# Kernel tuning notes

Measured on AMD Instinct MI355X. Metric: run time of the kernel, lower is better.

The kernel has to match this reference:

```python
import jax, jax.numpy as jnp
import numpy as np

B, D, A, R = 256, 1024, 1024, 8  # batch, feat_dim, ada_dim, rank
I = A  # inter_dim defaults to ada_dim
LN_EPS = 1e-5


def setup_inputs() -> dict:
    key = jax.random.key(0)
    ks = jax.random.split(key, 5)
    return {
        "x": jax.random.normal(ks[0], (B, D), jnp.float32),
        "ada_emb": jax.random.normal(ks[1], (B, A), jnp.float32),
        "base_layer": jax.random.normal(ks[2], (D, D), jnp.float32) * 0.02,
        "ln_gamma": jnp.ones((A,), jnp.float32),
        "ln_beta": jnp.zeros((A,), jnp.float32),
        "W1": jax.random.normal(ks[3], (A, I), jnp.float32) * 0.02,
        "b1": jnp.zeros((I,), jnp.float32),
        "W2": jax.random.normal(ks[4], (I, D * R * 2), jnp.float32) * 0.02,
        "b2": jnp.zeros((D * R * 2,), jnp.float32),
    }


def reference(x, ada_emb, base_layer, ln_gamma, ln_beta, W1, b1, W2, b2):
    Bc, Dc = x.shape
    # norm_cond: LayerNorm over ada_dim
    mu = jnp.mean(ada_emb, axis=-1, keepdims=True)
    var = jnp.var(ada_emb, axis=-1, keepdims=True)
    cond = (ada_emb - mu) * jax.lax.rsqrt(var + LN_EPS) * ln_gamma + ln_beta
    # gen_weight: Linear -> GELU (exact, erf) -> Linear
    h = jax.nn.gelu(cond @ W1 + b1, approximate=False)
    w = h @ W2 + b2                      # [B, 2*D*R]
    x_a, x_b = jnp.split(w, 2, axis=-1)
    x_a = x_a.reshape(Bc, Dc, R)         # [B, D, R]
    x_b = x_b.reshape(Bc, Dc, R)         # [B, D, R]
    # per-sample low-rank weight added to the shared base layer
    layer = base_layer[None, :, :] + jnp.einsum('bdr,bkr->bdk', x_a, x_b)  # [B, D, D]
    out = jnp.einsum('bc,bco->bo', x, layer)
    return x + out  # residual=True
```

## Files before the change

### kernel.cpp

```cpp
#include <hip/hip_runtime.h>
#include <math.h>

#define BB 256
#define DD 1024
#define AA 1024
#define RR 8
#define II 1024
#define NOUT (2*DD*RR)
#define LN_EPS 1e-5f

typedef __attribute__((ext_vector_type(8))) short bf16x8;
typedef __attribute__((ext_vector_type(8))) unsigned short ushort8;
typedef __attribute__((ext_vector_type(4))) float f32x4;

typedef const __attribute__((address_space(1))) unsigned int gu32_t;
typedef __attribute__((address_space(3))) unsigned int lu32_t;

__device__ __forceinline__ void glds16(void* lds, const void* g) {
    __builtin_amdgcn_global_load_lds((gu32_t*)g, (lu32_t*)lds, 16, 0, 0);
}

__device__ __forceinline__ f32x4 mfma16(bf16x8 a, bf16x8 b, f32x4 c) {
    return __builtin_amdgcn_mfma_f32_16x16x32_bf16(a, b, c, 0, 0, 0);
}

__device__ __forceinline__ unsigned short f2bf(float x) {
    unsigned int u = __float_as_uint(x);
    unsigned int r = (u + 0x7fffu + ((u >> 16) & 1u)) >> 16;
    return (unsigned short)r;
}
__device__ __forceinline__ float bf2f(unsigned short b) {
    return __uint_as_float(((unsigned int)b) << 16);
}
__device__ __forceinline__ void split2(float x, unsigned short& hi, unsigned short& lo) {
    hi = f2bf(x);
    lo = f2bf(x - bf2f(hi));
}

__device__ __forceinline__ float gelu_exact(float v) {
    return 0.5f * v * (1.0f + erff(v * 0.70710678118654752f));
}

__global__ __launch_bounds__(256) void ln_split_kernel(const float* __restrict__ ada,
                                                       const float* __restrict__ xp,
                                                       const float* __restrict__ gamma,
                                                       const float* __restrict__ beta,
                                                       unsigned short* __restrict__ c_hi,
                                                       unsigned short* __restrict__ c_lo,
                                                       unsigned short* __restrict__ x_hi,
                                                       unsigned short* __restrict__ x_lo) {
    const int b = blockIdx.x;
    const int tid = threadIdx.x;
    const float4 v = ((const float4*)(ada + (size_t)b * AA))[tid];

    float s  = v.x + v.y + v.z + v.w;
    float ss = v.x * v.x + v.y * v.y + v.z * v.z + v.w * v.w;
    #pragma unroll
    for (int off = 32; off; off >>= 1) {
        s  += __shfl_down(s, off);
        ss += __shfl_down(ss, off);
    }
    __shared__ float red[2][4];
    const int wid = tid >> 6, lane = tid & 63;
    if (lane == 0) { red[0][wid] = s; red[1][wid] = ss; }
    __syncthreads();
    __shared__ float stats[2];
    if (tid == 0) {
        float S  = red[0][0] + red[0][1] + red[0][2] + red[0][3];
        float SS = red[1][0] + red[1][1] + red[1][2] + red[1][3];
        float mu  = S * (1.0f / AA);
        float var = SS * (1.0f / AA) - mu * mu;
        stats[0] = mu;
        stats[1] = rsqrtf(var + LN_EPS);
    }
    __syncthreads();
    const float mu = stats[0], inv = stats[1];
    const float4 g  = ((const float4*)gamma)[tid];
    const float4 be = ((const float4*)beta)[tid];
    float o[4];
    o[0] = (v.x - mu) * inv * g.x + be.x;
    o[1] = (v.y - mu) * inv * g.y + be.y;
    o[2] = (v.z - mu) * inv * g.z + be.z;
    o[3] = (v.w - mu) * inv * g.w + be.w;
    ushort4 H, L;
    split2(o[0], H.x, L.x); split2(o[1], H.y, L.y);
    split2(o[2], H.z, L.z); split2(o[3], H.w, L.w);
    ((ushort4*)(c_hi + (size_t)b * AA))[tid] = H;
    ((ushort4*)(c_lo + (size_t)b * AA))[tid] = L;

    const float4 xv = ((const float4*)(xp + (size_t)b * DD))[tid];
    split2(xv.x, H.x, L.x); split2(xv.y, H.y, L.y);
    split2(xv.z, H.z, L.z); split2(xv.w, H.w, L.w);
    ((ushort4*)(x_hi + (size_t)b * DD))[tid] = H;
    ((ushort4*)(x_lo + (size_t)b * DD))[tid] = L;
}

__global__ __launch_bounds__(256) void gemm_small(const unsigned short* __restrict__ x_hi,
                                                  const unsigned short* __restrict__ x_lo,
                                                  const unsigned short* __restrict__ c_hi,
                                                  const unsigned short* __restrict__ c_lo,
                                                  const float* __restrict__ base,
                                                  const float* __restrict__ W1,
                                                  const float* __restrict__ b1,
                                                  float* __restrict__ outy,
                                                  unsigned short* __restrict__ h_hi,
                                                  unsigned short* __restrict__ h_lo) {
    __shared__ __align__(16) unsigned short As[2][4096];
    __shared__ __align__(16) unsigned short Bs[2][8192];

    const int z = blockIdx.z;
    const unsigned short* __restrict__ Ahi = z ? c_hi : x_hi;
    const unsigned short* __restrict__ Alo = z ? c_lo : x_lo;
    const float* __restrict__ Bsrc = z ? W1 : base;

    const int tid = threadIdx.x;
    const int bn = blockIdx.x * 64;
    const int bm = blockIdx.y * 32;
    const int wid = tid >> 6, l = tid & 63;
    const int kg = l >> 4, lr16 = (l & 15) * 16;

    f32x4 acc[2];
    acc[0] = (f32x4)0.0f; acc[1] = (f32x4)0.0f;

    const int sn = tid & 63;
    const int s_nb = sn >> 4, s_l16 = (sn & 15) * 16;

    float v[2][8];

    #define SB_LOAD(K0)                                                          \
        _Pragma("unroll")                                                        \
        for (int h = 0; h < 2; h++) {                                            \
            const int c2 = (tid >> 6) * 2 + h;              \
            _Pragma("unroll")                                                    \
            for (int j = 0; j < 8; j++)                                          \
                v[h][j] = Bsrc[(size_t)((K0) + c2 * 8 + j) * 1024 + bn + sn];    \
        }

    #define SB_WRITE(BUF)                                                        \
        _Pragma("unroll")                                                        \
        for (int h = 0; h < 2; h++) {                                            \
            const int c2 = (tid >> 6) * 2 + h;                                   \
            ushort8 H, L;                                                        \
            _Pragma("unroll")                                                    \
            for (int j = 0; j < 8; j++) { unsigned short hh, ll;                 \
                split2(v[h][j], hh, ll); H[j] = hh; L[j] = ll; }                 \
            *(ushort8*)((char*)Bs[BUF] + ((0*4 + s_nb)*8 + c2)*256 + s_l16) = H; \
            *(ushort8*)((char*)Bs[BUF] + ((1*4 + s_nb)*8 + c2)*256 + s_l16) = L; \
        }

    #define SA_GLDS(BUF, K0)                                                     \
        _Pragma("unroll")                                                        \
        for (int c = 0; c < 2; c++) {                                            \
            const int ch = wid * 2 + c;                                \
            const int pl = ch >> 2, sub = ch & 3;                                \
            const int mb = sub >> 1, half = sub & 1;                             \
            const unsigned short* src = (pl ? Alo : Ahi)                         \
                + (size_t)(bm + mb * 16 + (l & 15)) * 1024 + (K0) + half * 32 + kg * 8; \
            glds16((char*)As[BUF] + (pl*2 + mb)*2048 + half*1024, src);          \
        }

    #define S_COMPUTE(BUF)                                                       \
        {                                                                        \
            _Pragma("unroll")                                                    \
            for (int s = 0; s < 2; s++) {                                        \
                bf16x8 a[2][2], bbf[2];                                          \
                _Pragma("unroll")                                                \
                for (int pl = 0; pl < 2; pl++) {                                 \
                    _Pragma("unroll")                                            \
                    for (int mi = 0; mi < 2; mi++)                               \
                        a[pl][mi] = *(const bf16x8*)((const char*)As[BUF] +      \
                            ((pl*2 + mi)*8 + s*4 + kg)*256 + lr16);              \
                    bbf[pl] = *(const bf16x8*)((const char*)Bs[BUF] +            \
                            ((pl*4 + wid)*8 + s*4 + kg)*256 + lr16);             \
                }                                                                \
                __builtin_amdgcn_s_setprio(1);                                   \
                _Pragma("unroll")                                                \
                for (int mi = 0; mi < 2; mi++) {                                 \
                    acc[mi] = mfma16(a[0][mi], bbf[0], acc[mi]);                 \
                    acc[mi] = mfma16(a[0][mi], bbf[1], acc[mi]);                 \
                    acc[mi] = mfma16(a[1][mi], bbf[0], acc[mi]);                 \
                }                                                                \
                __builtin_amdgcn_s_setprio(0);                                   \
            }                                                                    \
        }

    SB_LOAD(0);
    SA_GLDS(0, 0);
    SB_WRITE(0);
    __syncthreads();

    int cur = 0;
    for (int t = 0; t < 16; ++t) {
        if (t < 15) {
            const int k0n = (t + 1) * 64;
            SB_LOAD(k0n);
            SA_GLDS(cur ^ 1, k0n);
        }
        S_COMPUTE(cur);
        if (t < 15) {
            SB_WRITE(cur ^ 1);
        }
        __syncthreads();
        cur ^= 1;
    }

    #pragma unroll
    for (int mi = 0; mi < 2; mi++) {
        const int row0 = bm + mi * 16 + kg * 4;
        const int col  = bn + wid * 16 + (l & 15);
        #pragma unroll
        for (int j = 0; j < 4; j++) {
            float val = acc[mi][j];
            if (z == 0) {
                outy[(size_t)(row0 + j) * 1024 + col] = val;
            } else {
                float g = gelu_exact(val + b1[col]);
                unsigned short hi, lo;
                split2(g, hi, lo);
                h_hi[(size_t)(row0 + j) * 1024 + col] = hi;
                h_lo[(size_t)(row0 + j) * 1024 + col] = lo;
            }
        }
    }
    #undef SB_LOAD
    #undef SB_WRITE
    #undef SA_GLDS
    #undef S_COMPUTE
}

__global__ __launch_bounds__(256) void gemm_big(const unsigned short* __restrict__ Ahi,
                                                const unsigned short* __restrict__ Alo,
                                                const float* __restrict__ Bm,
                                                const float* __restrict__ bias,
                                                float* __restrict__ Cm) {
    __shared__ __align__(16) unsigned short As[2][8192];
    __shared__ __align__(16) unsigned short Bs[2][4096];

    const int orig = blockIdx.x;
    const int swz  = ((orig & 7) << 6) + (orig >> 3);
    const int bn = (swz >> 1) * 64;
    const int bm = (swz & 1) * 128;

    const int tid = threadIdx.x;
    const int wid = tid >> 6, l = tid & 63;
    const int wm = wid >> 1, wn = wid & 1;
    const int kg = l >> 4, lr16 = (l & 15) * 16;

    f32x4 acc[4][2];
    #pragma unroll
    for (int i = 0; i < 4; i++) { acc[i][0] = (f32x4)0.0f; acc[i][1] = (f32x4)0.0f; }

    const int sn = tid & 63;
    const int skc = tid >> 6;
    const int s_nb = sn >> 4, s_l16 = (sn & 15) * 16;

    float v[8];

    #define GB_LOAD(K0)                                                          \
        _Pragma("unroll")                                                        \
        for (int j = 0; j < 8; j++)                                              \
            v[j] = Bm[(size_t)((K0) + skc * 8 + j) * NOUT + bn + sn];

    #define GB_WRITE(BUF)                                                        \
        {                                                                        \
            ushort8 H, L;                                                        \
            _Pragma("unroll")                                                    \
            for (int j = 0; j < 8; j++) { unsigned short hh, ll;                 \
                split2(v[j], hh, ll); H[j] = hh; L[j] = ll; }                    \
            *(ushort8*)((char*)Bs[BUF] + ((0*4 + s_nb)*4 + skc)*256 + s_l16) = H;\
            *(ushort8*)((char*)Bs[BUF] + ((1*4 + s_nb)*4 + skc)*256 + s_l16) = L;\
        }

    #define GA_GLDS(BUF, K0)                                                     \
        _Pragma("unroll")                                                        \
        for (int c = 0; c < 4; c++) {                                            \
            const int ch = wid * 4 + c;                               \
            const int pl = ch >> 3, mb = ch & 7;                                 \
            const unsigned short* src = (pl ? Alo : Ahi)                         \
                + (size_t)(bm + mb * 16 + (l & 15)) * II + (K0) + kg * 8;        \
            glds16((char*)As[BUF] + ch * 1024, src);                             \
        }

    #define G_COMPUTE(BUF)                                                       \
        {                                                                        \
            bf16x8 a[2][4], bbf[2][2];                                           \
            _Pragma("unroll")                                                    \
            for (int pl = 0; pl < 2; pl++) {                                     \
                _Pragma("unroll")                                                \
                for (int mi = 0; mi < 4; mi++)                                   \
                    a[pl][mi] = *(const bf16x8*)((const char*)As[BUF] +          \
                        ((pl*8 + wm*4 + mi)*4 + kg)*256 + lr16);                 \
                _Pragma("unroll")                                                \
                for (int ni = 0; ni < 2; ni++)                                   \
                    bbf[pl][ni] = *(const bf16x8*)((const char*)Bs[BUF] +        \
                        ((pl*4 + wn*2 + ni)*4 + kg)*256 + lr16);                 \
            }                                                                    \
            __builtin_amdgcn_s_setprio(1);                                       \
            _Pragma("unroll")                                                    \
            for (int mi = 0; mi < 4; mi++) {                                     \
                _Pragma("unroll")                                                \
                for (int ni = 0; ni < 2; ni++) {                                 \
                    acc[mi][ni] = mfma16(a[0][mi], bbf[0][ni], acc[mi][ni]);     \
                    acc[mi][ni] = mfma16(a[0][mi], bbf[1][ni], acc[mi][ni]);     \
                    acc[mi][ni] = mfma16(a[1][mi], bbf[0][ni], acc[mi][ni]);     \
                }                                                                \
            }                                                                    \
            __builtin_amdgcn_s_setprio(0);                                       \
        }

    GB_LOAD(0);
    GA_GLDS(0, 0);
    GB_WRITE(0);
    __syncthreads();

    int cur = 0;
    for (int t = 0; t < 32; ++t) {
        if (t < 31) {
            const int k0n = (t + 1) * 32;
            GB_LOAD(k0n);
            GA_GLDS(cur ^ 1, k0n);
        }
        G_COMPUTE(cur);
        if (t < 31) {
            GB_WRITE(cur ^ 1);
        }
        __syncthreads();
        cur ^= 1;
    }

    #pragma unroll
    for (int mi = 0; mi < 4; mi++) {
        #pragma unroll
        for (int ni = 0; ni < 2; ni++) {
            const int row0 = bm + wm * 64 + mi * 16 + kg * 4;
            const int col  = bn + wn * 32 + ni * 16 + (l & 15);
            const float bv = bias[col];
            #pragma unroll
            for (int j = 0; j < 4; j++)
                Cm[(size_t)(row0 + j) * NOUT + col] = acc[mi][ni][j] + bv;
        }
    }
    #undef GB_LOAD
    #undef GB_WRITE
    #undef GA_GLDS
    #undef G_COMPUTE
}

__global__ __launch_bounds__(256) void tail_kernel(const float* __restrict__ x,
                                                   const float* __restrict__ w,
                                                   float* __restrict__ out) {
    const int b = blockIdx.x;
    const int tid = threadIdx.x;
    const float* wa = w + (size_t)b * NOUT;
    const float4 xv = ((const float4*)(x + (size_t)b * DD))[tid];
    const float xs[4] = {xv.x, xv.y, xv.z, xv.w};

    float acc[RR] = {};
    #pragma unroll
    for (int i = 0; i < 4; i++) {
        const int c = tid * 4 + i;
        const float4 w0 = *(const float4*)&wa[c * RR];
        const float4 w1 = *(const float4*)&wa[c * RR + 4];
        acc[0] = fmaf(xs[i], w0.x, acc[0]);
        acc[1] = fmaf(xs[i], w0.y, acc[1]);
        acc[2] = fmaf(xs[i], w0.z, acc[2]);
        acc[3] = fmaf(xs[i], w0.w, acc[3]);
        acc[4] = fmaf(xs[i], w1.x, acc[4]);
        acc[5] = fmaf(xs[i], w1.y, acc[5]);
        acc[6] = fmaf(xs[i], w1.z, acc[6]);
        acc[7] = fmaf(xs[i], w1.w, acc[7]);
    }
    __shared__ float red[4][RR];
    __shared__ float trs[RR];
    const int wid = tid >> 6, lane = tid & 63;
    #pragma unroll
    for (int r = 0; r < RR; r++) {
        float vv = acc[r];
        #pragma unroll
        for (int off = 32; off; off >>= 1) vv += __shfl_down(vv, off);
        if (lane == 0) red[wid][r] = vv;
    }
    __syncthreads();
    if (tid < RR) trs[tid] = red[0][tid] + red[1][tid] + red[2][tid] + red[3][tid];
    __syncthreads();

    float tr[RR];
    #pragma unroll
    for (int r = 0; r < RR; r++) tr[r] = trs[r];

    const float* wb = wa + DD * RR;
    const int o0 = tid * 4;
    const float4 yv = *(const float4*)&out[(size_t)b * DD + o0];

    float vals[4];
    #pragma unroll
    for (int i = 0; i < 4; i++) {
        const float4 w0 = *(const float4*)&wb[(o0 + i) * RR];
        const float4 w1 = *(const float4*)&wb[(o0 + i) * RR + 4];
        vals[i] = tr[0] * w0.x + tr[1] * w0.y + tr[2] * w0.z + tr[3] * w0.w
                + tr[4] * w1.x + tr[5] * w1.y + tr[6] * w1.z + tr[7] * w1.w;
    }
    float4 o;
    o.x = xv.x + yv.x + vals[0];
    o.y = xv.y + yv.y + vals[1];
    o.z = xv.z + yv.z + vals[2];
    o.w = xv.w + yv.w + vals[3];
    *(float4*)&out[(size_t)b * DD + o0] = o;
}

extern "C" void kernel_launch(void* const* d_in, const int* in_sizes, int n_in,
                              void* d_out, int out_size, void* d_ws, size_t ws_size,
                              hipStream_t stream) {
    const float* x     = (const float*)d_in[0];
    const float* ada   = (const float*)d_in[1];
    const float* base  = (const float*)d_in[2];
    const float* gamma = (const float*)d_in[3];
    const float* beta  = (const float*)d_in[4];
    const float* W1    = (const float*)d_in[5];
    const float* b1    = (const float*)d_in[6];
    const float* W2    = (const float*)d_in[7];
    const float* b2    = (const float*)d_in[8];
    float* out = (float*)d_out;

    char* wsb = (char*)d_ws;
    float* w = (float*)(wsb);
    unsigned short* h_hi = (unsigned short*)(wsb + 16777216);
    unsigned short* h_lo = (unsigned short*)(wsb + 17301504);
    unsigned short* x_hi = (unsigned short*)(wsb + 17825792);
    unsigned short* x_lo = (unsigned short*)(wsb + 18350080);
    unsigned short* c_hi = (unsigned short*)(wsb + 18874368);
    unsigned short* c_lo = (unsigned short*)(wsb + 19398656);

    ln_split_kernel<<<BB, 256, 0, stream>>>(ada, x, gamma, beta, c_hi, c_lo, x_hi, x_lo);

    gemm_small<<<dim3(1024 / 64, BB / 32, 2), 256, 0, stream>>>(
        x_hi, x_lo, c_hi, c_lo, base, W1, b1, out, h_hi, h_lo);

    gemm_big<<<512, 256, 0, stream>>>(h_hi, h_lo, W2, b2, w);

    tail_kernel<<<BB, 256, 0, stream>>>(x, w, out);
}
```

Measured before the change: 186.5 us.

## Pre-tile split activations in MFMA layout and enlarge big GEMM tiles

The LayerNorm and GELU epilogues now write the bf16 hi/lo split activations directly into an MFMA-ready tiled image, so the GEMMs load A tiles with contiguous global_load_lds copies. gemm_big moves to 128x128 tiles with 512 threads and a 2D grid, replacing the swizzled 64x128 blocks. Both GEMM loops swap __syncthreads for explicit waitcnt and barrier regions. This costs scattered 2-byte stores in the GELU epilogue, a larger LDS footprint, and the loss of the block swizzle for L2 locality.

```diff
diff --git a/kernel.cpp b/kernel.cpp
--- a/kernel.cpp
+++ b/kernel.cpp
@@ -41,14 +41,23 @@
     return 0.5f * v * (1.0f + erff(v * 0.70710678118654752f));
 }
 
+__device__ __forceinline__ void region_top_wait() {
+    asm volatile("s_waitcnt vmcnt(0) lgkmcnt(0)" ::: "memory");
+    __builtin_amdgcn_sched_barrier(0);
+    __builtin_amdgcn_s_barrier();
+    __builtin_amdgcn_sched_barrier(0);
+}
+__device__ __forceinline__ void region_end_wait() {
+    asm volatile("s_waitcnt lgkmcnt(0)" ::: "memory");
+    __builtin_amdgcn_sched_barrier(0);
+}
+
 __global__ __launch_bounds__(256) void ln_split_kernel(const float* __restrict__ ada,
                                                        const float* __restrict__ xp,
                                                        const float* __restrict__ gamma,
                                                        const float* __restrict__ beta,
-                                                       unsigned short* __restrict__ c_hi,
-                                                       unsigned short* __restrict__ c_lo,
-                                                       unsigned short* __restrict__ x_hi,
-                                                       unsigned short* __restrict__ x_lo) {
+                                                       char* __restrict__ c_t,
+                                                       char* __restrict__ x_t) {
     const int b = blockIdx.x;
     const int tid = threadIdx.x;
     const float4 v = ((const float4*)(ada + (size_t)b * AA))[tid];
@@ -77,6 +86,12 @@
     const float mu = stats[0], inv = stats[1];
     const float4 g  = ((const float4*)gamma)[tid];
     const float4 be = ((const float4*)beta)[tid];
+
+    const int k0 = tid * 4;
+    const int mbh = (b >> 4) & 1;
+    const size_t img = ((size_t)(b >> 5) * 16 + (k0 >> 6)) * 8192;
+    const int inoff = ((k0 >> 3) & 7) * 256 + (b & 15) * 16 + (k0 & 7) * 2;
+
     float o[4];
     o[0] = (v.x - mu) * inv * g.x + be.x;
     o[1] = (v.y - mu) * inv * g.y + be.y;
@@ -85,32 +100,28 @@
     ushort4 H, L;
     split2(o[0], H.x, L.x); split2(o[1], H.y, L.y);
     split2(o[2], H.z, L.z); split2(o[3], H.w, L.w);
-    ((ushort4*)(c_hi + (size_t)b * AA))[tid] = H;
-    ((ushort4*)(c_lo + (size_t)b * AA))[tid] = L;
+    *(ushort4*)(c_t + img + (0 * 2 + mbh) * 2048 + inoff) = H;
+    *(ushort4*)(c_t + img + (1 * 2 + mbh) * 2048 + inoff) = L;
 
     const float4 xv = ((const float4*)(xp + (size_t)b * DD))[tid];
     split2(xv.x, H.x, L.x); split2(xv.y, H.y, L.y);
     split2(xv.z, H.z, L.z); split2(xv.w, H.w, L.w);
-    ((ushort4*)(x_hi + (size_t)b * DD))[tid] = H;
-    ((ushort4*)(x_lo + (size_t)b * DD))[tid] = L;
-}
-
-__global__ __launch_bounds__(256) void gemm_small(const unsigned short* __restrict__ x_hi,
-                                                  const unsigned short* __restrict__ x_lo,
-                                                  const unsigned short* __restrict__ c_hi,
-                                                  const unsigned short* __restrict__ c_lo,
+    *(ushort4*)(x_t + img + (0 * 2 + mbh) * 2048 + inoff) = H;
+    *(ushort4*)(x_t + img + (1 * 2 + mbh) * 2048 + inoff) = L;
+}
+
+__global__ __launch_bounds__(256) void gemm_small(const char* __restrict__ x_t,
+                                                  const char* __restrict__ c_t,
                                                   const float* __restrict__ base,
                                                   const float* __restrict__ W1,
                                                   const float* __restrict__ b1,
                                                   float* __restrict__ outy,
-                                                  unsigned short* __restrict__ h_hi,
-                                                  unsigned short* __restrict__ h_lo) {
-    __shared__ __align__(16) unsigned short As[2][4096];
-    __shared__ __align__(16) unsigned short Bs[2][8192];
+                                                  char* __restrict__ h_t) {
+    __shared__ __align__(16) char As[2][8192];
+    __shared__ __align__(16) char Bs[2][16384];
 
     const int z = blockIdx.z;
-    const unsigned short* __restrict__ Ahi = z ? c_hi : x_hi;
-    const unsigned short* __restrict__ Alo = z ? c_lo : x_lo;
+    const char* __restrict__ At = z ? c_t : x_t;
     const float* __restrict__ Bsrc = z ? W1 : base;
 
     const int tid = threadIdx.x;
@@ -123,85 +134,75 @@
     acc[0] = (f32x4)0.0f; acc[1] = (f32x4)0.0f;
 
     const int sn = tid & 63;
+    const int sk0 = (tid >> 6) * 16;
     const int s_nb = sn >> 4, s_l16 = (sn & 15) * 16;
 
-    float v[2][8];
-
-    #define SB_LOAD(K0)                                                          \
+    float v[16];
+
+    #define SB_LOAD(KT)                                                          \
         _Pragma("unroll")                                                        \
-        for (int h = 0; h < 2; h++) {                                            \
-            const int c2 = (tid >> 6) * 2 + h;              \
-            _Pragma("unroll")                                                    \
-            for (int j = 0; j < 8; j++)                                          \
-                v[h][j] = Bsrc[(size_t)((K0) + c2 * 8 + j) * 1024 + bn + sn];    \
-        }
+        for (int j = 0; j < 16; j++)                                             \
+            v[j] = Bsrc[(size_t)((KT) * 64 + sk0 + j) * 1024 + bn + sn];
 
     #define SB_WRITE(BUF)                                                        \
         _Pragma("unroll")                                                        \
-        for (int h = 0; h < 2; h++) {                                            \
-            const int c2 = (tid >> 6) * 2 + h;                                   \
+        for (int h2 = 0; h2 < 2; h2++) {                                         \
+            const int kidx = (sk0 >> 3) + h2;                                    \
             ushort8 H, L;                                                        \
             _Pragma("unroll")                                                    \
             for (int j = 0; j < 8; j++) { unsigned short hh, ll;                 \
-                split2(v[h][j], hh, ll); H[j] = hh; L[j] = ll; }                 \
-            *(ushort8*)((char*)Bs[BUF] + ((0*4 + s_nb)*8 + c2)*256 + s_l16) = H; \
-            *(ushort8*)((char*)Bs[BUF] + ((1*4 + s_nb)*8 + c2)*256 + s_l16) = L; \
-        }
-
-    #define SA_GLDS(BUF, K0)                                                     \
+                split2(v[h2 * 8 + j], hh, ll); H[j] = hh; L[j] = ll; }           \
+            *(ushort8*)(Bs[BUF] + ((0*4 + s_nb)*8 + kidx)*256 + s_l16) = H;      \
+            *(ushort8*)(Bs[BUF] + ((1*4 + s_nb)*8 + kidx)*256 + s_l16) = L;      \
+        }
+
+    #define SA_GLDS(BUF, KT)                                                     \
+        {                                                                        \
+            const char* ib = At + ((size_t)(bm >> 5) * 16 + (KT)) * 8192;        \
+            _Pragma("unroll")                                                    \
+            for (int c = 0; c < 2; c++) {                                        \
+                const int ch = wid * 2 + c;                                      \
+                glds16(As[BUF] + ch * 1024, ib + ch * 1024 + l * 16);            \
+            }                                                                    \
+        }
+
+    #define S_COMPUTE(BUF)                                                       \
         _Pragma("unroll")                                                        \
-        for (int c = 0; c < 2; c++) {                                            \
-            const int ch = wid * 2 + c;                                \
-            const int pl = ch >> 2, sub = ch & 3;                                \
-            const int mb = sub >> 1, half = sub & 1;                             \
-            const unsigned short* src = (pl ? Alo : Ahi)                         \
-                + (size_t)(bm + mb * 16 + (l & 15)) * 1024 + (K0) + half * 32 + kg * 8; \
-            glds16((char*)As[BUF] + (pl*2 + mb)*2048 + half*1024, src);          \
-        }
-
-    #define S_COMPUTE(BUF)                                                       \
-        {                                                                        \
-            _Pragma("unroll")                                                    \
-            for (int s = 0; s < 2; s++) {                                        \
-                bf16x8 a[2][2], bbf[2];                                          \
+        for (int s2 = 0; s2 < 2; s2++) {                                         \
+            bf16x8 a[2][2], bbf[2];                                              \
+            _Pragma("unroll")                                                    \
+            for (int pl = 0; pl < 2; pl++) {                                     \
                 _Pragma("unroll")                                                \
-                for (int pl = 0; pl < 2; pl++) {                                 \
-                    _Pragma("unroll")                                            \
-                    for (int mi = 0; mi < 2; mi++)                               \
-                        a[pl][mi] = *(const bf16x8*)((const char*)As[BUF] +      \
-                            ((pl*2 + mi)*8 + s*4 + kg)*256 + lr16);              \
-                    bbf[pl] = *(const bf16x8*)((const char*)Bs[BUF] +            \
-                            ((pl*4 + wid)*8 + s*4 + kg)*256 + lr16);             \
-                }                                                                \
-                __builtin_amdgcn_s_setprio(1);                                   \
-                _Pragma("unroll")                                                \
-                for (int mi = 0; mi < 2; mi++) {                                 \
-                    acc[mi] = mfma16(a[0][mi], bbf[0], acc[mi]);                 \
-                    acc[mi] = mfma16(a[0][mi], bbf[1], acc[mi]);                 \
-                    acc[mi] = mfma16(a[1][mi], bbf[0], acc[mi]);                 \
-                }                                                                \
-                __builtin_amdgcn_s_setprio(0);                                   \
+                for (int mi = 0; mi < 2; mi++)                                   \
+                    a[pl][mi] = *(const bf16x8*)(As[BUF] +                       \
+                        ((pl*2 + mi)*8 + s2*4 + kg)*256 + lr16);                 \
+                bbf[pl] = *(const bf16x8*)(Bs[BUF] +                             \
+                        ((pl*4 + wid)*8 + s2*4 + kg)*256 + lr16);                \
+            }                                                                    \
+            _Pragma("unroll")                                                    \
+            for (int mi = 0; mi < 2; mi++) {                                     \
+                acc[mi] = mfma16(a[0][mi], bbf[0], acc[mi]);                     \
+                acc[mi] = mfma16(a[0][mi], bbf[1], acc[mi]);                     \
+                acc[mi] = mfma16(a[1][mi], bbf[0], acc[mi]);                     \
             }                                                                    \
         }
 
     SB_LOAD(0);
     SA_GLDS(0, 0);
     SB_WRITE(0);
-    __syncthreads();
-
-    int cur = 0;
+
     for (int t = 0; t < 16; ++t) {
+        const int cur = t & 1;
+        region_top_wait();
         if (t < 15) {
-            const int k0n = (t + 1) * 64;
-            SB_LOAD(k0n);
-            SA_GLDS(cur ^ 1, k0n);
+            SB_LOAD(t + 1);
+            SA_GLDS(cur ^ 1, t + 1);
         }
         S_COMPUTE(cur);
         if (t < 15) {
             SB_WRITE(cur ^ 1);
         }
-        __syncthreads();
-        cur ^= 1;
+        region_end_wait();
     }
 
     #pragma unroll
@@ -211,14 +212,18 @@
         #pragma unroll
         for (int j = 0; j < 4; j++) {
             float val = acc[mi][j];
+            const int row = row0 + j;
             if (z == 0) {
-                outy[(size_t)(row0 + j) * 1024 + col] = val;
+                outy[(size_t)row * 1024 + col] = val;
             } else {
                 float g = gelu_exact(val + b1[col]);
                 unsigned short hi, lo;
                 split2(g, hi, lo);
-                h_hi[(size_t)(row0 + j) * 1024 + col] = hi;
-                h_lo[(size_t)(row0 + j) * 1024 + col] = lo;
+                char* ib = h_t + ((size_t)(row >> 7) * 32 + (col >> 5)) * 16384;
+                const int inoff = (((row >> 4) & 7) * 4 + ((col >> 3) & 3)) * 256
+                                + (row & 15) * 16 + (col & 7) * 2;
+                *(unsigned short*)(ib + 0 * 8192 + inoff) = hi;
+                *(unsigned short*)(ib + 1 * 8192 + inoff) = lo;
             }
         }
     }
@@ -228,38 +233,34 @@
     #undef S_COMPUTE
 }
 
-__global__ __launch_bounds__(256) void gemm_big(const unsigned short* __restrict__ Ahi,
-                                                const unsigned short* __restrict__ Alo,
+__global__ __launch_bounds__(512) void gemm_big(const char* __restrict__ h_t,
                                                 const float* __restrict__ Bm,
                                                 const float* __restrict__ bias,
                                                 float* __restrict__ Cm) {
-    __shared__ __align__(16) unsigned short As[2][8192];
-    __shared__ __align__(16) unsigned short Bs[2][4096];
-
-    const int orig = blockIdx.x;
-    const int swz  = ((orig & 7) << 6) + (orig >> 3);
-    const int bn = (swz >> 1) * 64;
-    const int bm = (swz & 1) * 128;
+    __shared__ __align__(16) char As[2][16384];
+    __shared__ __align__(16) char Bs[2][16384];
 
     const int tid = threadIdx.x;
+    const int bn = blockIdx.x * 128;
+    const int bm = blockIdx.y * 128;
     const int wid = tid >> 6, l = tid & 63;
-    const int wm = wid >> 1, wn = wid & 1;
+    const int wm = wid >> 2, wn = wid & 3;
     const int kg = l >> 4, lr16 = (l & 15) * 16;
 
     f32x4 acc[4][2];
     #pragma unroll
     for (int i = 0; i < 4; i++) { acc[i][0] = (f32x4)0.0f; acc[i][1] = (f32x4)0.0f; }
 
-    const int sn = tid & 63;
-    const int skc = tid >> 6;
+    const int sn = tid & 127;
+    const int skg = tid >> 7;
     const int s_nb = sn >> 4, s_l16 = (sn & 15) * 16;
 
     float v[8];
 
-    #define GB_LOAD(K0)                                                          \
+    #define GB_LOAD(KT)                                                          \
         _Pragma("unroll")                                                        \
         for (int j = 0; j < 8; j++)                                              \
-            v[j] = Bm[(size_t)((K0) + skc * 8 + j) * NOUT + bn + sn];
+            v[j] = Bm[(size_t)((KT) * 32 + skg * 8 + j) * NOUT + bn + sn];
 
     #define GB_WRITE(BUF)                                                        \
         {                                                                        \
@@ -267,18 +268,18 @@
             _Pragma("unroll")                                                    \
             for (int j = 0; j < 8; j++) { unsigned short hh, ll;                 \
                 split2(v[j], hh, ll); H[j] = hh; L[j] = ll; }                    \
-            *(ushort8*)((char*)Bs[BUF] + ((0*4 + s_nb)*4 + skc)*256 + s_l16) = H;\
-            *(ushort8*)((char*)Bs[BUF] + ((1*4 + s_nb)*4 + skc)*256 + s_l16) = L;\
-        }
-
-    #define GA_GLDS(BUF, K0)                                                     \
-        _Pragma("unroll")                                                        \
-        for (int c = 0; c < 4; c++) {                                            \
-            const int ch = wid * 4 + c;                               \
-            const int pl = ch >> 3, mb = ch & 7;                                 \
-            const unsigned short* src = (pl ? Alo : Ahi)                         \
-                + (size_t)(bm + mb * 16 + (l & 15)) * II + (K0) + kg * 8;        \
-            glds16((char*)As[BUF] + ch * 1024, src);                             \
+            *(ushort8*)(Bs[BUF] + ((0*8 + s_nb)*4 + skg)*256 + s_l16) = H;       \
+            *(ushort8*)(Bs[BUF] + ((1*8 + s_nb)*4 + skg)*256 + s_l16) = L;       \
+        }
+
+    #define GA_GLDS(BUF, KT)                                                     \
+        {                                                                        \
+            const char* ib = h_t + ((size_t)(bm >> 7) * 32 + (KT)) * 16384;      \
+            _Pragma("unroll")                                                    \
+            for (int c = 0; c < 2; c++) {                                        \
+                const int ch = wid * 2 + c;                                      \
+                glds16(As[BUF] + ch * 1024, ib + ch * 1024 + l * 16);            \
+            }                                                                    \
         }
 
     #define G_COMPUTE(BUF)                                                       \
@@ -288,12 +289,12 @@
             for (int pl = 0; pl < 2; pl++) {                                     \
                 _Pragma("unroll")                                                \
                 for (int mi = 0; mi < 4; mi++)                                   \
-                    a[pl][mi] = *(const bf16x8*)((const char*)As[BUF] +          \
+                    a[pl][mi] = *(const bf16x8*)(As[BUF] +                       \
                         ((pl*8 + wm*4 + mi)*4 + kg)*256 + lr16);                 \
                 _Pragma("unroll")                                                \
                 for (int ni = 0; ni < 2; ni++)                                   \
-                    bbf[pl][ni] = *(const bf16x8*)((const char*)Bs[BUF] +        \
-                        ((pl*4 + wn*2 + ni)*4 + kg)*256 + lr16);                 \
+                    bbf[pl][ni] = *(const bf16x8*)(Bs[BUF] +                     \
+                        ((pl*8 + wn*2 + ni)*4 + kg)*256 + lr16);                 \
             }                                                                    \
             __builtin_amdgcn_s_setprio(1);                                       \
             _Pragma("unroll")                                                    \
@@ -311,21 +312,19 @@
     GB_LOAD(0);
     GA_GLDS(0, 0);
     GB_WRITE(0);
-    __syncthreads();
-
-    int cur = 0;
+
     for (int t = 0; t < 32; ++t) {
+        const int cur = t & 1;
+        region_top_wait();
         if (t < 31) {
-            const int k0n = (t + 1) * 32;
-            GB_LOAD(k0n);
-            GA_GLDS(cur ^ 1, k0n);
+            GB_LOAD(t + 1);
+            GA_GLDS(cur ^ 1, t + 1);
         }
         G_COMPUTE(cur);
         if (t < 31) {
             GB_WRITE(cur ^ 1);
         }
-        __syncthreads();
-        cur ^= 1;
+        region_end_wait();
     }
 
     #pragma unroll
@@ -423,20 +422,17 @@
     float* out = (float*)d_out;
 
     char* wsb = (char*)d_ws;
-    float* w = (float*)(wsb);
-    unsigned short* h_hi = (unsigned short*)(wsb + 16777216);
-    unsigned short* h_lo = (unsigned short*)(wsb + 17301504);
-    unsigned short* x_hi = (unsigned short*)(wsb + 17825792);
-    unsigned short* x_lo = (unsigned short*)(wsb + 18350080);
-    unsigned short* c_hi = (unsigned short*)(wsb + 18874368);
-    unsigned short* c_lo = (unsigned short*)(wsb + 19398656);
-
-    ln_split_kernel<<<BB, 256, 0, stream>>>(ada, x, gamma, beta, c_hi, c_lo, x_hi, x_lo);
+    float* w  = (float*)(wsb);
+    char* h_t = wsb + 16777216;
+    char* x_t = wsb + 17825792;
+    char* c_t = wsb + 18874368;
+
+    ln_split_kernel<<<BB, 256, 0, stream>>>(ada, x, gamma, beta, c_t, x_t);
 
     gemm_small<<<dim3(1024 / 64, BB / 32, 2), 256, 0, stream>>>(
-        x_hi, x_lo, c_hi, c_lo, base, W1, b1, out, h_hi, h_lo);
-
-    gemm_big<<<512, 256, 0, stream>>>(h_hi, h_lo, W2, b2, w);
+        x_t, c_t, base, W1, b1, out, h_t);
+
+    gemm_big<<<dim3(NOUT / 128, BB / 128), 512, 0, stream>>>(h_t, W2, b2, w);
 
     tail_kernel<<<BB, 256, 0, stream>>>(x, w, out);
 }
```

New measurement: 178.0 us. -4.6%, faster.
